# Optimization experiments

Measured on AMD Instinct MI355X. Metric: run time of the kernel, lower is better.

Reference implementation:

```python
import jax, jax.numpy as jnp
import numpy as np
from jax import lax

PATCH_SIZE = 7
NEIGH_SIZE = 9
SIGMA = 2.0
EPS = 1e-05


def _gaussian_kernel(sigma, sz):
    mid = sz // 2
    ax = np.arange(sz) - mid
    g = np.exp(-(ax[:, None] ** 2 + ax[None, :] ** 2) / (2.0 * sigma ** 2)) / (2.0 * np.pi * sigma ** 2)
    return g.astype(np.float32)


KERNEL = jnp.asarray(_gaussian_kernel(SIGMA, PATCH_SIZE))[None, None]  # (1,1,7,7)

_half = NEIGH_SIZE // 2
SHIFTS = jnp.asarray(
    [(x, y) for x in range(-_half, NEIGH_SIZE - _half)
     for y in range(-_half, NEIGH_SIZE - _half) if (x, y) != (0, 0)],
    dtype=jnp.int32)  # (80, 2) — xshift outer loop, yshift inner, matching torch order
SHIFTS4 = jnp.asarray([(-1, 0), (1, 0), (0, -1), (0, 1)], dtype=jnp.int32)


def _translate(img, tx, ty):
    # Faithful to torch affine_grid + grid_sample(nearest, zeros, align_corners=False):
    # a 'translation' of tx in normalized coords samples input at pixel j + tx*W/2.
    # H, W even and tx, ty integers -> exact integer pixel shifts, zero padding.
    H, W = img.shape
    px = jnp.arange(W) + tx * (W // 2)
    py = jnp.arange(H) + ty * (H // 2)
    mask = ((py >= 0) & (py < H))[:, None] & ((px >= 0) & (px < W))[None, :]
    out = img[jnp.clip(py, 0, H - 1)[:, None], jnp.clip(px, 0, W - 1)[None, :]]
    return jnp.where(mask, out, jnp.zeros((), img.dtype))


def _blur(x):
    # x: (N, H, W); conv2d with gaussian kernel, stride 1, padding 3 (same for 7x7)
    y = lax.conv_general_dilated(x[:, None], KERNEL, (1, 1), [(3, 3), (3, 3)],
                                 dimension_numbers=('NCHW', 'OIHW', 'NCHW'))
    return y[:, 0]


def _dp_batch(img2d, shifts):
    # Dp for a batch of shifts: shift, diff, square, gaussian blur
    shifted = jax.vmap(lambda s: _translate(img2d, s[0], s[1]))(shifts)  # (N,H,W)
    return _blur((img2d[None] - shifted) ** 2)


def setup_inputs() -> dict:
    key = jax.random.key(0)
    k1, k2 = jax.random.split(key)
    image1 = jax.random.normal(k1, (1, 1, 1024, 1024), dtype=jnp.float32)
    image2 = jax.random.normal(k2, (1, 1, 1024, 1024), dtype=jnp.float32)
    return {"image1": image1, "image2": image2}


def reference(image1, image2):
    img1 = image1[0, 0]  # (H, W)
    img2 = image2[0, 0]
    H, W = img1.shape
    reduce_size = (PATCH_SIZE + NEIGH_SIZE - 2) // 2  # = 7
    # Vimg: average of 4 single-pixel-neighborhood Dp's on image1, + eps
    Vimg = _dp_batch(img1, SHIFTS4).sum(axis=0) / 4.0 + EPS  # (H, W)
    # 80-shift MIND responses on image2
    D2 = _dp_batch(img2, SHIFTS)  # (80, H, W)
    mind = jnp.exp(-D2 / Vimg[None])
    # torch slices: dim1 end index is (C - reduce_size) = 1-7 = -6 -> H-6;
    # dim2 end index is (H - reduce_size). Replicated exactly (H == W).
    out = mind[:, reduce_size:H + 1 - reduce_size, reduce_size:H - reduce_size]
    mx = jnp.max(out, axis=0)
    return jnp.mean(out / mx[None])
```

## Files before the change

kernel.cpp:

```cpp
#include <hip/hip_runtime.h>
#include <cmath>

#define IMG_W 1024
#define SROWS 22
#define SCOLS 73

struct GK { float gh[7]; float gv[7]; };

__device__ __forceinline__ float warp_block_sum(float v, float* wsum, int tx, int ty) {
    #pragma unroll
    for (int off = 32; off > 0; off >>= 1)
        v += __shfl_down(v, off, 64);
    if (tx == 0) wsum[ty] = v;
    __syncthreads();
    return wsum[0] + wsum[1] + wsum[2] + wsum[3];
}

__global__ __launch_bounds__(256)
void mind_tile(const float* __restrict__ img1, const float* __restrict__ img2,
               float* __restrict__ partials, GK gk)
{
    __shared__ float4 s1[SROWS * SCOLS];

    const int tx  = (int)threadIdx.x;
    const int ty  = (int)threadIdx.y;
    const int tid = ty * 64 + tx;
    const int x0  = 7 + 64 * (int)blockIdx.x;
    const int y0  = 7 + 16 * (int)blockIdx.y;
    const int x4  = x0 - 3;

    #pragma unroll 2
    for (int it = tid; it < SROWS * 18; it += 256) {
        const int r   = it / 18;
        const int j   = it - r * 18;
        const int sr  = min(y0 - 3 + r, 1023);
        const int srp = sr ^ 512;
        const int scc = min(x4 + 4 * j, 1020);
        const int scp = scc ^ 512;
        const float4 a  = *(const float4*)&img2[sr  * IMG_W + scc];
        const float4 b  = *(const float4*)&img2[sr  * IMG_W + scp];
        const float4 c2 = *(const float4*)&img2[srp * IMG_W + scc];
        const float4 d  = *(const float4*)&img2[srp * IMG_W + scp];
        const float4 u  = *(const float4*)&img1[sr  * IMG_W + scc];
        const float4 ub = *(const float4*)&img1[sr  * IMG_W + scp];
        const float4 uc = *(const float4*)&img1[srp * IMG_W + scc];
        float4* __restrict__ dst = &s1[r * SCOLS + 4 * j];
        #define MIND_FIELD(E, K) { \
            const float a2 = a.E * a.E; \
            const float tb = a.E - b.E, tc = a.E - c2.E, td = a.E - d.E; \
            const float su = u.E - ub.E, sv = u.E - uc.E; \
            float4 f; \
            f.x = fmaf(tb, tb, -a2);                            \
            f.y = fmaf(tc, tc, -a2);                            \
            f.z = fmaf(td, td, -a2);                            \
            f.w = fmaf(u.E, u.E + u.E, fmaf(su, su, sv * sv));  \
            dst[K] = f; }
        MIND_FIELD(x, 0)
        MIND_FIELD(y, 1)
        MIND_FIELD(z, 2)
        MIND_FIELD(w, 3)
        #undef MIND_FIELD
    }
    __syncthreads();

    const bool xs = (x0 - 3 <= 511) && (x0 + 66 >= 512);
    const bool ys = (y0 - 3 <= 511) && (y0 + 18 >= 512);
    const bool xok = (x0 + tx <= 1016);
    float tsum = 0.f;

    if (!xs && !ys) {
        float Px[4] = {0,0,0,0}, Py[4] = {0,0,0,0}, Pd[4] = {0,0,0,0}, V4[4] = {0,0,0,0};
        #pragma unroll
        for (int r = 0; r < 10; ++r) {
            const float4* __restrict__ row = &s1[(4 * ty + r) * SCOLS + tx];
            float hH = 0, hV = 0, hD = 0, hU = 0;
            #pragma unroll
            for (int kx = 0; kx < 7; ++kx) {
                const float4 g = row[kx];
                hH = fmaf(gk.gh[kx], g.x, hH);
                hV = fmaf(gk.gh[kx], g.y, hV);
                hD = fmaf(gk.gh[kx], g.z, hD);
                hU = fmaf(gk.gh[kx], g.w, hU);
            }
            #pragma unroll
            for (int o = 0; o < 4; ++o) {
                if (r - o >= 0 && r - o <= 6) {
                    const float g = gk.gv[r - o];
                    Px[o] = fmaf(g, hH, Px[o]);
                    Py[o] = fmaf(g, hV, Py[o]);
                    Pd[o] = fmaf(g, hD, Pd[o]);
                    V4[o] = fmaf(g, hU, V4[o]);
                }
            }
        }
        #pragma unroll
        for (int o = 0; o < 4; ++o) {
            const float V = fmaf(V4[o], 0.25f, 1e-5f);
            const float invV = 1.0f / V;
            float M = fminf(0.f, Px[o]);
            M = fminf(M, Py[o]); M = fminf(M, Pd[o]);
            const float pix = 77.f * __expf(M * invV)
                + __expf((M - Px[o]) * invV)
                + __expf((M - Py[o]) * invV)
                + __expf((M - Pd[o]) * invV);
            const bool ok = xok && (y0 + 4 * ty + o <= 1017);
            tsum += ok ? pix : 0.f;
        }
    } else {
        float glx[7], ghx[7];
        #pragma unroll
        for (int kx = 0; kx < 7; ++kx) {
            const bool lo = (((x0 - 3 + tx + kx) & 512) == 0);
            glx[kx] = lo ? gk.gh[kx] : 0.f;
            ghx[kx] = lo ? 0.f : gk.gh[kx];
        }
        float Ph[4]  = {0,0,0,0}, Qh[4]  = {0,0,0,0}, Pv[4] = {0,0,0,0}, Qv[4] = {0,0,0,0};
        float Ppp[4] = {0,0,0,0}, Ppm[4] = {0,0,0,0}, Pmp[4] = {0,0,0,0}, Pmm[4] = {0,0,0,0};
        float V4[4]  = {0,0,0,0};
        #pragma unroll
        for (int r = 0; r < 10; ++r) {
            const float4* __restrict__ row = &s1[(4 * ty + r) * SCOLS + tx];
            float hHlo = 0, hHhi = 0, hV = 0, hDlo = 0, hDhi = 0, hU = 0;
            #pragma unroll
            for (int kx = 0; kx < 7; ++kx) {
                const float4 g = row[kx];
                hHlo = fmaf(glx[kx],   g.x, hHlo);
                hHhi = fmaf(ghx[kx],   g.x, hHhi);
                hV   = fmaf(gk.gh[kx], g.y, hV);
                hDlo = fmaf(glx[kx],   g.z, hDlo);
                hDhi = fmaf(ghx[kx],   g.z, hDhi);
                hU   = fmaf(gk.gh[kx], g.w, hU);
            }
            const bool ylo = (((y0 + 4 * ty - 3 + r) & 512) == 0);
            #pragma unroll
            for (int o = 0; o < 4; ++o) {
                if (r - o >= 0 && r - o <= 6) {
                    const float g  = gk.gv[r - o];
                    const float wl = ylo ? g : 0.f;
                    const float wh = ylo ? 0.f : g;
                    Ph [o] = fmaf(g,  hHlo, Ph [o]);
                    Qh [o] = fmaf(g,  hHhi, Qh [o]);
                    Pv [o] = fmaf(wl, hV,   Pv [o]);
                    Qv [o] = fmaf(wh, hV,   Qv [o]);
                    Ppp[o] = fmaf(wl, hDlo, Ppp[o]);
                    Ppm[o] = fmaf(wh, hDlo, Ppm[o]);
                    Pmp[o] = fmaf(wl, hDhi, Pmp[o]);
                    Pmm[o] = fmaf(wh, hDhi, Pmm[o]);
                    V4 [o] = fmaf(g,  hU,   V4 [o]);
                }
            }
        }
        #pragma unroll
        for (int o = 0; o < 4; ++o) {
            const float V = fmaf(V4[o], 0.25f, 1e-5f);
            const float invV = 1.0f / V;
            float M = fminf(0.f, Ph[o]);
            M = fminf(M, Qh[o]);  M = fminf(M, Pv[o]);  M = fminf(M, Qv[o]);
            M = fminf(M, Ppp[o]); M = fminf(M, Pmp[o]); M = fminf(M, Ppm[o]); M = fminf(M, Pmm[o]);
            const float pix = 72.f * __expf(M * invV)
                + __expf((M - Ph [o]) * invV) + __expf((M - Qh [o]) * invV)
                + __expf((M - Pv [o]) * invV) + __expf((M - Qv [o]) * invV)
                + __expf((M - Ppp[o]) * invV) + __expf((M - Pmp[o]) * invV)
                + __expf((M - Ppm[o]) * invV) + __expf((M - Pmm[o]) * invV);
            const bool ok = xok && (y0 + 4 * ty + o <= 1017);
            tsum += ok ? pix : 0.f;
        }
    }

    __shared__ float wsum[4];
    const float bt = warp_block_sum(tsum, wsum, tx, ty);
    if (tid == 0)
        partials[(int)blockIdx.y * gridDim.x + (int)blockIdx.x] = bt;
}

__global__ __launch_bounds__(256)
void mind_reduce(const float* __restrict__ partials, float* __restrict__ out)
{
    float s = 0.f;
    #pragma unroll
    for (int k = 0; k < 4; ++k)
        s += partials[(int)threadIdx.x + 256 * k];
    double d = (double)s;
    #pragma unroll
    for (int off = 32; off > 0; off >>= 1)
        d += __shfl_down(d, off, 64);
    __shared__ double sm[4];
    const int lane = (int)threadIdx.x & 63, wid = (int)threadIdx.x >> 6;
    if (lane == 0) sm[wid] = d;
    __syncthreads();
    if (threadIdx.x == 0)
        out[0] = (float)((sm[0] + sm[1] + sm[2] + sm[3]) / 81688800.0);
}

extern "C" void kernel_launch(void* const* d_in, const int* in_sizes, int n_in,
                              void* d_out, int out_size, void* d_ws, size_t ws_size,
                              hipStream_t stream) {
    const float* img1 = (const float*)d_in[0];
    const float* img2 = (const float*)d_in[1];
    float* out = (float*)d_out;
    float* partials = (float*)d_ws;

    GK gk;
    for (int i = 0; i < 7; ++i) {
        const double dv = i - 3;
        gk.gh[i] = (float)std::exp(-(dv * dv) / 8.0);
        gk.gv[i] = (float)(std::exp(-(dv * dv) / 8.0) / (8.0 * M_PI));
    }

    dim3 block(64, 4);
    dim3 grid(16, 64);
    mind_tile<<<grid, block, 0, stream>>>(img1, img2, partials, gk);
    mind_reduce<<<1, 256, 0, stream>>>(partials, out);
}
```

Measured before the change: 70.06 us.

## Double tile height, compute two columns per thread, swizzle shared layout

```diff
diff --git a/kernel.cpp b/kernel.cpp
--- a/kernel.cpp
+++ b/kernel.cpp
@@ -2,10 +2,14 @@
 #include <cmath>
 
 #define IMG_W 1024
-#define SROWS 22
-#define SCOLS 73
+#define SROWS 38
+#define SCST  73
+#define NCHUNK 18
+#define NITEMS (SROWS * NCHUNK)
 
 struct GK { float gh[7]; float gv[7]; };
+
+__device__ __forceinline__ int swz(int c) { return c ^ ((c >> 3) & 7); }
 
 __device__ __forceinline__ float warp_block_sum(float v, float* wsum, int tx, int ty) {
     #pragma unroll
@@ -16,154 +20,187 @@
     return wsum[0] + wsum[1] + wsum[2] + wsum[3];
 }
 
-__global__ __launch_bounds__(256)
+__global__ __launch_bounds__(256, 2)
 void mind_tile(const float* __restrict__ img1, const float* __restrict__ img2,
                float* __restrict__ partials, GK gk)
 {
-    __shared__ float4 s1[SROWS * SCOLS];
+    __shared__ float4 s1[SROWS * SCST];
 
     const int tx  = (int)threadIdx.x;
     const int ty  = (int)threadIdx.y;
     const int tid = ty * 64 + tx;
     const int x0  = 7 + 64 * (int)blockIdx.x;
-    const int y0  = 7 + 16 * (int)blockIdx.y;
+    const int y0  = 7 + 32 * (int)blockIdx.y;
     const int x4  = x0 - 3;
 
-    #pragma unroll 2
-    for (int it = tid; it < SROWS * 18; it += 256) {
-        const int r   = it / 18;
-        const int j   = it - r * 18;
-        const int sr  = min(y0 - 3 + r, 1023);
-        const int srp = sr ^ 512;
-        const int scc = min(x4 + 4 * j, 1020);
-        const int scp = scc ^ 512;
-        const float4 a  = *(const float4*)&img2[sr  * IMG_W + scc];
-        const float4 b  = *(const float4*)&img2[sr  * IMG_W + scp];
-        const float4 c2 = *(const float4*)&img2[srp * IMG_W + scc];
-        const float4 d  = *(const float4*)&img2[srp * IMG_W + scp];
-        const float4 u  = *(const float4*)&img1[sr  * IMG_W + scc];
-        const float4 ub = *(const float4*)&img1[sr  * IMG_W + scp];
-        const float4 uc = *(const float4*)&img1[srp * IMG_W + scc];
-        float4* __restrict__ dst = &s1[r * SCOLS + 4 * j];
-        #define MIND_FIELD(E, K) { \
-            const float a2 = a.E * a.E; \
-            const float tb = a.E - b.E, tc = a.E - c2.E, td = a.E - d.E; \
-            const float su = u.E - ub.E, sv = u.E - uc.E; \
-            float4 f; \
-            f.x = fmaf(tb, tb, -a2);                            \
-            f.y = fmaf(tc, tc, -a2);                            \
-            f.z = fmaf(td, td, -a2);                            \
-            f.w = fmaf(u.E, u.E + u.E, fmaf(su, su, sv * sv));  \
-            dst[K] = f; }
-        MIND_FIELD(x, 0)
-        MIND_FIELD(y, 1)
-        MIND_FIELD(z, 2)
-        MIND_FIELD(w, 3)
-        #undef MIND_FIELD
+    #pragma unroll
+    for (int ii = 0; ii < 3; ++ii) {
+        const int it = tid + 256 * ii;
+        if (it < NITEMS) {
+            const int r   = it / NCHUNK;
+            const int j   = it - r * NCHUNK;
+            const int sr  = min(y0 - 3 + r, 1023);
+            const int srp = sr ^ 512;
+            const int scc = min(x4 + 4 * j, 1020);
+            const int scp = scc ^ 512;
+            const float4 a  = *(const float4*)&img2[sr  * IMG_W + scc];
+            const float4 b  = *(const float4*)&img2[sr  * IMG_W + scp];
+            const float4 c2 = *(const float4*)&img2[srp * IMG_W + scc];
+            const float4 d  = *(const float4*)&img2[srp * IMG_W + scp];
+            const float4 u  = *(const float4*)&img1[sr  * IMG_W + scc];
+            const float4 ub = *(const float4*)&img1[sr  * IMG_W + scp];
+            const float4 uc = *(const float4*)&img1[srp * IMG_W + scc];
+            float4* __restrict__ dst = &s1[r * SCST];
+            #define MIND_FIELD(E, K) { \
+                const float a2 = a.E * a.E; \
+                const float tb = a.E - b.E, tc = a.E - c2.E, td = a.E - d.E; \
+                const float su = u.E - ub.E, sv = u.E - uc.E; \
+                float4 f; \
+                f.x = fmaf(tb, tb, -a2);                            \
+                f.y = fmaf(tc, tc, -a2);                            \
+                f.z = fmaf(td, td, -a2);                            \
+                f.w = fmaf(u.E, u.E + u.E, fmaf(su, su, sv * sv));  \
+                dst[swz(4 * j + K)] = f; }
+            MIND_FIELD(x, 0)
+            MIND_FIELD(y, 1)
+            MIND_FIELD(z, 2)
+            MIND_FIELD(w, 3)
+            #undef MIND_FIELD
+        }
     }
     __syncthreads();
 
     const bool xs = (x0 - 3 <= 511) && (x0 + 66 >= 512);
-    const bool ys = (y0 - 3 <= 511) && (y0 + 18 >= 512);
-    const bool xok = (x0 + tx <= 1016);
+    const bool ys = (y0 - 3 <= 511) && (y0 + 34 >= 512);
+
+    const int s_    = tx & 31;
+    const int rg    = 2 * ty + (tx >> 5);
+    const int colg0 = x0 + 2 * s_;
+    int coff[8];
+    #pragma unroll
+    for (int k = 0; k < 8; ++k) coff[k] = swz(2 * s_ + k);
+
     float tsum = 0.f;
 
     if (!xs && !ys) {
-        float Px[4] = {0,0,0,0}, Py[4] = {0,0,0,0}, Pd[4] = {0,0,0,0}, V4[4] = {0,0,0,0};
+        float Px[2][4] = {{0}}, Py[2][4] = {{0}}, Pd[2][4] = {{0}}, V4[2][4] = {{0}};
         #pragma unroll
         for (int r = 0; r < 10; ++r) {
-            const float4* __restrict__ row = &s1[(4 * ty + r) * SCOLS + tx];
-            float hH = 0, hV = 0, hD = 0, hU = 0;
-            #pragma unroll
-            for (int kx = 0; kx < 7; ++kx) {
-                const float4 g = row[kx];
-                hH = fmaf(gk.gh[kx], g.x, hH);
-                hV = fmaf(gk.gh[kx], g.y, hV);
-                hD = fmaf(gk.gh[kx], g.z, hD);
-                hU = fmaf(gk.gh[kx], g.w, hU);
-            }
+            const int rowbase = (4 * rg + r) * SCST;
+            float4 f[8];
+            #pragma unroll
+            for (int k = 0; k < 8; ++k) f[k] = s1[rowbase + coff[k]];
+            #pragma unroll
+            for (int cc = 0; cc < 2; ++cc) {
+                float hH = 0, hV = 0, hD = 0, hU = 0;
+                #pragma unroll
+                for (int k = 0; k < 7; ++k) {
+                    const float4 g = f[k + cc];
+                    hH = fmaf(gk.gh[k], g.x, hH);
+                    hV = fmaf(gk.gh[k], g.y, hV);
+                    hD = fmaf(gk.gh[k], g.z, hD);
+                    hU = fmaf(gk.gh[k], g.w, hU);
+                }
+                #pragma unroll
+                for (int o = 0; o < 4; ++o) {
+                    if (r - o >= 0 && r - o <= 6) {
+                        const float g = gk.gv[r - o];
+                        Px[cc][o] = fmaf(g, hH, Px[cc][o]);
+                        Py[cc][o] = fmaf(g, hV, Py[cc][o]);
+                        Pd[cc][o] = fmaf(g, hD, Pd[cc][o]);
+                        V4[cc][o] = fmaf(g, hU, V4[cc][o]);
+                    }
+                }
+            }
+        }
+        #pragma unroll
+        for (int cc = 0; cc < 2; ++cc) {
+            const bool xok = (colg0 + cc <= 1016);
             #pragma unroll
             for (int o = 0; o < 4; ++o) {
-                if (r - o >= 0 && r - o <= 6) {
-                    const float g = gk.gv[r - o];
-                    Px[o] = fmaf(g, hH, Px[o]);
-                    Py[o] = fmaf(g, hV, Py[o]);
-                    Pd[o] = fmaf(g, hD, Pd[o]);
-                    V4[o] = fmaf(g, hU, V4[o]);
-                }
-            }
-        }
-        #pragma unroll
-        for (int o = 0; o < 4; ++o) {
-            const float V = fmaf(V4[o], 0.25f, 1e-5f);
-            const float invV = 1.0f / V;
-            float M = fminf(0.f, Px[o]);
-            M = fminf(M, Py[o]); M = fminf(M, Pd[o]);
-            const float pix = 77.f * __expf(M * invV)
-                + __expf((M - Px[o]) * invV)
-                + __expf((M - Py[o]) * invV)
-                + __expf((M - Pd[o]) * invV);
-            const bool ok = xok && (y0 + 4 * ty + o <= 1017);
-            tsum += ok ? pix : 0.f;
+                const float V = fmaf(V4[cc][o], 0.25f, 1e-5f);
+                const float invV = 1.0f / V;
+                float M = fminf(0.f, Px[cc][o]);
+                M = fminf(M, Py[cc][o]); M = fminf(M, Pd[cc][o]);
+                const float pix = 77.f * __expf(M * invV)
+                    + __expf((M - Px[cc][o]) * invV)
+                    + __expf((M - Py[cc][o]) * invV)
+                    + __expf((M - Pd[cc][o]) * invV);
+                const bool ok = xok && (y0 + 4 * rg + o <= 1017);
+                tsum += ok ? pix : 0.f;
+            }
         }
     } else {
-        float glx[7], ghx[7];
-        #pragma unroll
-        for (int kx = 0; kx < 7; ++kx) {
-            const bool lo = (((x0 - 3 + tx + kx) & 512) == 0);
-            glx[kx] = lo ? gk.gh[kx] : 0.f;
-            ghx[kx] = lo ? 0.f : gk.gh[kx];
-        }
-        float Ph[4]  = {0,0,0,0}, Qh[4]  = {0,0,0,0}, Pv[4] = {0,0,0,0}, Qv[4] = {0,0,0,0};
-        float Ppp[4] = {0,0,0,0}, Ppm[4] = {0,0,0,0}, Pmp[4] = {0,0,0,0}, Pmm[4] = {0,0,0,0};
-        float V4[4]  = {0,0,0,0};
+        float glx[2][7], ghx[2][7];
+        #pragma unroll
+        for (int cc = 0; cc < 2; ++cc)
+            #pragma unroll
+            for (int k = 0; k < 7; ++k) {
+                const bool lo = (((x4 + 2 * s_ + cc + k) & 512) == 0);
+                glx[cc][k] = lo ? gk.gh[k] : 0.f;
+                ghx[cc][k] = lo ? 0.f : gk.gh[k];
+            }
+        float Ph[2][4]  = {{0}}, Qh[2][4]  = {{0}}, Pv[2][4] = {{0}}, Qv[2][4] = {{0}};
+        float Ppp[2][4] = {{0}}, Ppm[2][4] = {{0}}, Pmp[2][4] = {{0}}, Pmm[2][4] = {{0}};
+        float V4[2][4]  = {{0}};
         #pragma unroll
         for (int r = 0; r < 10; ++r) {
-            const float4* __restrict__ row = &s1[(4 * ty + r) * SCOLS + tx];
-            float hHlo = 0, hHhi = 0, hV = 0, hDlo = 0, hDhi = 0, hU = 0;
-            #pragma unroll
-            for (int kx = 0; kx < 7; ++kx) {
-                const float4 g = row[kx];
-                hHlo = fmaf(glx[kx],   g.x, hHlo);
-                hHhi = fmaf(ghx[kx],   g.x, hHhi);
-                hV   = fmaf(gk.gh[kx], g.y, hV);
-                hDlo = fmaf(glx[kx],   g.z, hDlo);
-                hDhi = fmaf(ghx[kx],   g.z, hDhi);
-                hU   = fmaf(gk.gh[kx], g.w, hU);
-            }
-            const bool ylo = (((y0 + 4 * ty - 3 + r) & 512) == 0);
+            const int rowbase = (4 * rg + r) * SCST;
+            float4 f[8];
+            #pragma unroll
+            for (int k = 0; k < 8; ++k) f[k] = s1[rowbase + coff[k]];
+            const bool ylo = (((y0 + 4 * rg - 3 + r) & 512) == 0);
+            #pragma unroll
+            for (int cc = 0; cc < 2; ++cc) {
+                float hHlo = 0, hHhi = 0, hV = 0, hDlo = 0, hDhi = 0, hU = 0;
+                #pragma unroll
+                for (int k = 0; k < 7; ++k) {
+                    const float4 g = f[k + cc];
+                    hHlo = fmaf(glx[cc][k], g.x, hHlo);
+                    hHhi = fmaf(ghx[cc][k], g.x, hHhi);
+                    hV   = fmaf(gk.gh[k],   g.y, hV);
+                    hDlo = fmaf(glx[cc][k], g.z, hDlo);
+                    hDhi = fmaf(ghx[cc][k], g.z, hDhi);
+                    hU   = fmaf(gk.gh[k],   g.w, hU);
+                }
+                #pragma unroll
+                for (int o = 0; o < 4; ++o) {
+                    if (r - o >= 0 && r - o <= 6) {
+                        const float g  = gk.gv[r - o];
+                        const float wl = ylo ? g : 0.f;
+                        const float wh = ylo ? 0.f : g;
+                        Ph [cc][o] = fmaf(g,  hHlo, Ph [cc][o]);
+                        Qh [cc][o] = fmaf(g,  hHhi, Qh [cc][o]);
+                        Pv [cc][o] = fmaf(wl, hV,   Pv [cc][o]);
+                        Qv [cc][o] = fmaf(wh, hV,   Qv [cc][o]);
+                        Ppp[cc][o] = fmaf(wl, hDlo, Ppp[cc][o]);
+                        Ppm[cc][o] = fmaf(wh, hDlo, Ppm[cc][o]);
+                        Pmp[cc][o] = fmaf(wl, hDhi, Pmp[cc][o]);
+                        Pmm[cc][o] = fmaf(wh, hDhi, Pmm[cc][o]);
+                        V4 [cc][o] = fmaf(g,  hU,   V4 [cc][o]);
+                    }
+                }
+            }
+        }
+        #pragma unroll
+        for (int cc = 0; cc < 2; ++cc) {
+            const bool xok = (colg0 + cc <= 1016);
             #pragma unroll
             for (int o = 0; o < 4; ++o) {
-                if (r - o >= 0 && r - o <= 6) {
-                    const float g  = gk.gv[r - o];
-                    const float wl = ylo ? g : 0.f;
-                    const float wh = ylo ? 0.f : g;
-                    Ph [o] = fmaf(g,  hHlo, Ph [o]);
-                    Qh [o] = fmaf(g,  hHhi, Qh [o]);
-                    Pv [o] = fmaf(wl, hV,   Pv [o]);
-                    Qv [o] = fmaf(wh, hV,   Qv [o]);
-                    Ppp[o] = fmaf(wl, hDlo, Ppp[o]);
-                    Ppm[o] = fmaf(wh, hDlo, Ppm[o]);
-                    Pmp[o] = fmaf(wl, hDhi, Pmp[o]);
-                    Pmm[o] = fmaf(wh, hDhi, Pmm[o]);
-                    V4 [o] = fmaf(g,  hU,   V4 [o]);
-                }
-            }
-        }
-        #pragma unroll
-        for (int o = 0; o < 4; ++o) {
-            const float V = fmaf(V4[o], 0.25f, 1e-5f);
-            const float invV = 1.0f / V;
-            float M = fminf(0.f, Ph[o]);
-            M = fminf(M, Qh[o]);  M = fminf(M, Pv[o]);  M = fminf(M, Qv[o]);
-            M = fminf(M, Ppp[o]); M = fminf(M, Pmp[o]); M = fminf(M, Ppm[o]); M = fminf(M, Pmm[o]);
-            const float pix = 72.f * __expf(M * invV)
-                + __expf((M - Ph [o]) * invV) + __expf((M - Qh [o]) * invV)
-                + __expf((M - Pv [o]) * invV) + __expf((M - Qv [o]) * invV)
-                + __expf((M - Ppp[o]) * invV) + __expf((M - Pmp[o]) * invV)
-                + __expf((M - Ppm[o]) * invV) + __expf((M - Pmm[o]) * invV);
-            const bool ok = xok && (y0 + 4 * ty + o <= 1017);
-            tsum += ok ? pix : 0.f;
+                const float V = fmaf(V4[cc][o], 0.25f, 1e-5f);
+                const float invV = 1.0f / V;
+                float M = fminf(0.f, Ph[cc][o]);
+                M = fminf(M, Qh[cc][o]);  M = fminf(M, Pv[cc][o]);  M = fminf(M, Qv[cc][o]);
+                M = fminf(M, Ppp[cc][o]); M = fminf(M, Pmp[cc][o]);
+                M = fminf(M, Ppm[cc][o]); M = fminf(M, Pmm[cc][o]);
+                const float pix = 72.f * __expf(M * invV)
+                    + __expf((M - Ph [cc][o]) * invV) + __expf((M - Qh [cc][o]) * invV)
+                    + __expf((M - Pv [cc][o]) * invV) + __expf((M - Qv [cc][o]) * invV)
+                    + __expf((M - Ppp[cc][o]) * invV) + __expf((M - Pmp[cc][o]) * invV)
+                    + __expf((M - Ppm[cc][o]) * invV) + __expf((M - Pmm[cc][o]) * invV);
+                const bool ok = xok && (y0 + 4 * rg + o <= 1017);
+                tsum += ok ? pix : 0.f;
+            }
         }
     }
 
@@ -176,10 +213,7 @@
 __global__ __launch_bounds__(256)
 void mind_reduce(const float* __restrict__ partials, float* __restrict__ out)
 {
-    float s = 0.f;
-    #pragma unroll
-    for (int k = 0; k < 4; ++k)
-        s += partials[(int)threadIdx.x + 256 * k];
+    float s = partials[(int)threadIdx.x] + partials[(int)threadIdx.x + 256];
     double d = (double)s;
     #pragma unroll
     for (int off = 32; off > 0; off >>= 1)
@@ -208,7 +242,7 @@
     }
 
     dim3 block(64, 4);
-    dim3 grid(16, 64);
+    dim3 grid(16, 32);
     mind_tile<<<grid, block, 0, stream>>>(img1, img2, partials, gk);
     mind_reduce<<<1, 256, 0, stream>>>(partials, out);
 }
```

Measured after the change: 110.7 us. 1.58x slower.

## Precompute horizontal blur once per row in shared memory with swizzled layout

Applied to the files above, without the earlier changes.

```diff
diff --git a/kernel.cpp b/kernel.cpp
--- a/kernel.cpp
+++ b/kernel.cpp
@@ -3,9 +3,13 @@
 
 #define IMG_W 1024
 #define SROWS 22
-#define SCOLS 73
+#define SCST  73
+#define NCHUNK 18
+#define NITEMS (SROWS * NCHUNK)
 
 struct GK { float gh[7]; float gv[7]; };
+
+__device__ __forceinline__ int swz(int c) { return c ^ ((c >> 3) & 7); }
 
 __device__ __forceinline__ float warp_block_sum(float v, float* wsum, int tx, int ty) {
     #pragma unroll
@@ -20,76 +24,105 @@
 void mind_tile(const float* __restrict__ img1, const float* __restrict__ img2,
                float* __restrict__ partials, GK gk)
 {
-    __shared__ float4 s1[SROWS * SCOLS];
+    __shared__ float4 s1[SROWS * SCST];
 
     const int tx  = (int)threadIdx.x;
     const int ty  = (int)threadIdx.y;
     const int tid = ty * 64 + tx;
-    const int x0  = 7 + 64 * (int)blockIdx.x;
-    const int y0  = 7 + 16 * (int)blockIdx.y;
+    const int bx  = ((int)blockIdx.x + 7)  & 15;
+    const int by  = ((int)blockIdx.y + 31) & 63;
+    const int x0  = 7 + 64 * bx;
+    const int y0  = 7 + 16 * by;
     const int x4  = x0 - 3;
 
-    #pragma unroll 2
-    for (int it = tid; it < SROWS * 18; it += 256) {
-        const int r   = it / 18;
-        const int j   = it - r * 18;
-        const int sr  = min(y0 - 3 + r, 1023);
-        const int srp = sr ^ 512;
-        const int scc = min(x4 + 4 * j, 1020);
-        const int scp = scc ^ 512;
-        const float4 a  = *(const float4*)&img2[sr  * IMG_W + scc];
-        const float4 b  = *(const float4*)&img2[sr  * IMG_W + scp];
-        const float4 c2 = *(const float4*)&img2[srp * IMG_W + scc];
-        const float4 d  = *(const float4*)&img2[srp * IMG_W + scp];
-        const float4 u  = *(const float4*)&img1[sr  * IMG_W + scc];
-        const float4 ub = *(const float4*)&img1[sr  * IMG_W + scp];
-        const float4 uc = *(const float4*)&img1[srp * IMG_W + scc];
-        float4* __restrict__ dst = &s1[r * SCOLS + 4 * j];
-        #define MIND_FIELD(E, K) { \
-            const float a2 = a.E * a.E; \
-            const float tb = a.E - b.E, tc = a.E - c2.E, td = a.E - d.E; \
-            const float su = u.E - ub.E, sv = u.E - uc.E; \
-            float4 f; \
-            f.x = fmaf(tb, tb, -a2);                            \
-            f.y = fmaf(tc, tc, -a2);                            \
-            f.z = fmaf(td, td, -a2);                            \
-            f.w = fmaf(u.E, u.E + u.E, fmaf(su, su, sv * sv));  \
-            dst[K] = f; }
-        MIND_FIELD(x, 0)
-        MIND_FIELD(y, 1)
-        MIND_FIELD(z, 2)
-        MIND_FIELD(w, 3)
-        #undef MIND_FIELD
+    #pragma unroll
+    for (int ii = 0; ii < 2; ++ii) {
+        const int it = tid + 256 * ii;
+        if (it < NITEMS) {
+            const int r   = it / NCHUNK;
+            const int j   = it - r * NCHUNK;
+            const int sr  = min(y0 - 3 + r, 1023);
+            const int srp = sr ^ 512;
+            const int scc = min(x4 + 4 * j, 1020);
+            const int scp = scc ^ 512;
+            const float4 a  = *(const float4*)&img2[sr  * IMG_W + scc];
+            const float4 b  = *(const float4*)&img2[sr  * IMG_W + scp];
+            const float4 c2 = *(const float4*)&img2[srp * IMG_W + scc];
+            const float4 d  = *(const float4*)&img2[srp * IMG_W + scp];
+            const float4 u  = *(const float4*)&img1[sr  * IMG_W + scc];
+            const float4 ub = *(const float4*)&img1[sr  * IMG_W + scp];
+            const float4 uc = *(const float4*)&img1[srp * IMG_W + scc];
+            float4* __restrict__ dst = &s1[r * SCST];
+            #define MIND_FIELD(E, K) { \
+                const float a2 = a.E * a.E; \
+                const float tb = a.E - b.E, tc = a.E - c2.E, td = a.E - d.E; \
+                const float su = u.E - ub.E, sv = u.E - uc.E; \
+                float4 f; \
+                f.x = fmaf(tb, tb, -a2);                            \
+                f.y = fmaf(tc, tc, -a2);                            \
+                f.z = fmaf(td, td, -a2);                            \
+                f.w = fmaf(u.E, u.E + u.E, fmaf(su, su, sv * sv));  \
+                dst[swz(4 * j + K)] = f; }
+            MIND_FIELD(x, 0)
+            MIND_FIELD(y, 1)
+            MIND_FIELD(z, 2)
+            MIND_FIELD(w, 3)
+            #undef MIND_FIELD
+        }
     }
     __syncthreads();
 
     const bool xs = (x0 - 3 <= 511) && (x0 + 66 >= 512);
     const bool ys = (y0 - 3 <= 511) && (y0 + 18 >= 512);
+    const bool straddle = xs || ys;
+
+    float4 hv[8];
+    const int brow = tid >> 3, bseg = tid & 7;
+    const bool btask = (!straddle) && (tid < 176);
+    if (btask) {
+        const float4* __restrict__ rb = &s1[brow * SCST];
+        float4 f[14];
+        #pragma unroll
+        for (int q = 0; q < 14; ++q) f[q] = rb[swz(8 * bseg + q)];
+        #pragma unroll
+        for (int o = 0; o < 8; ++o) {
+            float hH = 0, hV = 0, hD = 0, hU = 0;
+            #pragma unroll
+            for (int k = 0; k < 7; ++k) {
+                const float4 g = f[o + k];
+                hH = fmaf(gk.gh[k], g.x, hH);
+                hV = fmaf(gk.gh[k], g.y, hV);
+                hD = fmaf(gk.gh[k], g.z, hD);
+                hU = fmaf(gk.gh[k], g.w, hU);
+            }
+            hv[o] = make_float4(hH, hV, hD, hU);
+        }
+    }
+    __syncthreads();
+    if (btask) {
+        float4* __restrict__ rb = &s1[brow * SCST];
+        #pragma unroll
+        for (int o = 0; o < 8; ++o) rb[swz(8 * bseg + o)] = hv[o];
+    }
+    __syncthreads();
+
     const bool xok = (x0 + tx <= 1016);
     float tsum = 0.f;
 
-    if (!xs && !ys) {
+    if (!straddle) {
+        const int ci = swz(tx);
         float Px[4] = {0,0,0,0}, Py[4] = {0,0,0,0}, Pd[4] = {0,0,0,0}, V4[4] = {0,0,0,0};
         #pragma unroll
         for (int r = 0; r < 10; ++r) {
-            const float4* __restrict__ row = &s1[(4 * ty + r) * SCOLS + tx];
-            float hH = 0, hV = 0, hD = 0, hU = 0;
-            #pragma unroll
-            for (int kx = 0; kx < 7; ++kx) {
-                const float4 g = row[kx];
-                hH = fmaf(gk.gh[kx], g.x, hH);
-                hV = fmaf(gk.gh[kx], g.y, hV);
-                hD = fmaf(gk.gh[kx], g.z, hD);
-                hU = fmaf(gk.gh[kx], g.w, hU);
-            }
+            const float4 h = s1[(4 * ty + r) * SCST + ci];
             #pragma unroll
             for (int o = 0; o < 4; ++o) {
                 if (r - o >= 0 && r - o <= 6) {
                     const float g = gk.gv[r - o];
-                    Px[o] = fmaf(g, hH, Px[o]);
-                    Py[o] = fmaf(g, hV, Py[o]);
-                    Pd[o] = fmaf(g, hD, Pd[o]);
-                    V4[o] = fmaf(g, hU, V4[o]);
+                    Px[o] = fmaf(g, h.x, Px[o]);
+                    Py[o] = fmaf(g, h.y, Py[o]);
+                    Pd[o] = fmaf(g, h.z, Pd[o]);
+                    V4[o] = fmaf(g, h.w, V4[o]);
                 }
             }
         }
@@ -108,22 +141,24 @@
         }
     } else {
         float glx[7], ghx[7];
+        int cidx[7];
         #pragma unroll
         for (int kx = 0; kx < 7; ++kx) {
             const bool lo = (((x0 - 3 + tx + kx) & 512) == 0);
             glx[kx] = lo ? gk.gh[kx] : 0.f;
             ghx[kx] = lo ? 0.f : gk.gh[kx];
+            cidx[kx] = swz(tx + kx);
         }
         float Ph[4]  = {0,0,0,0}, Qh[4]  = {0,0,0,0}, Pv[4] = {0,0,0,0}, Qv[4] = {0,0,0,0};
         float Ppp[4] = {0,0,0,0}, Ppm[4] = {0,0,0,0}, Pmp[4] = {0,0,0,0}, Pmm[4] = {0,0,0,0};
         float V4[4]  = {0,0,0,0};
         #pragma unroll
         for (int r = 0; r < 10; ++r) {
-            const float4* __restrict__ row = &s1[(4 * ty + r) * SCOLS + tx];
+            const float4* __restrict__ row = &s1[(4 * ty + r) * SCST];
             float hHlo = 0, hHhi = 0, hV = 0, hDlo = 0, hDhi = 0, hU = 0;
             #pragma unroll
             for (int kx = 0; kx < 7; ++kx) {
-                const float4 g = row[kx];
+                const float4 g = row[cidx[kx]];
                 hHlo = fmaf(glx[kx],   g.x, hHlo);
                 hHhi = fmaf(ghx[kx],   g.x, hHhi);
                 hV   = fmaf(gk.gh[kx], g.y, hV);
@@ -170,7 +205,7 @@
     __shared__ float wsum[4];
     const float bt = warp_block_sum(tsum, wsum, tx, ty);
     if (tid == 0)
-        partials[(int)blockIdx.y * gridDim.x + (int)blockIdx.x] = bt;
+        partials[by * 16 + bx] = bt;
 }
 
 __global__ __launch_bounds__(256)
```

After: 70.42 us. Within noise of the previous version (+0.5%).
